# Kernel tuning notes

Hardware: AMD Instinct MI355X
Metric: run time of the kernel (lower is better)

Reference implementation:

```python
import jax, jax.numpy as jnp
import numpy as np

N, E = 50000, 800000
IN_DIM, HIDDEN, LATENT = 128, 256, 64


def setup_inputs() -> dict:
    key = jax.random.key(0)
    ks = jax.random.split(key, 10)
    def lin(k, fan_in, fan_out):
        s = 1.0 / np.sqrt(fan_in)
        return jax.random.uniform(k, (fan_in, fan_out), jnp.float32, -s, s)
    x = jax.random.normal(ks[0], (N, IN_DIM), jnp.float32)
    edge_index = jax.random.randint(ks[1], (2, E), 0, N, jnp.int64)
    return {
        "x": x,
        "edge_index": edge_index,
        # enc1: SAGEConv(in_dim, hidden): lin_l (neighbors, with bias), lin_r (root, no bias)
        "W1l": lin(ks[2], IN_DIM, HIDDEN),
        "b1": jnp.zeros((HIDDEN,), jnp.float32),
        "W1r": lin(ks[3], IN_DIM, HIDDEN),
        # enc2: SAGEConv(hidden, latent)
        "W2l": lin(ks[4], HIDDEN, LATENT),
        "b2": jnp.zeros((LATENT,), jnp.float32),
        "W2r": lin(ks[5], HIDDEN, LATENT),
        # decoder Linear(latent, in_dim)
        "Wd": lin(ks[6], LATENT, IN_DIM),
        "bd": jax.random.uniform(ks[7], (IN_DIM,), jnp.float32, -1.0 / np.sqrt(LATENT), 1.0 / np.sqrt(LATENT)),
    }


def _sage_conv(x, src, dst, Wl, b, Wr, num_nodes):
    # PyG SAGEConv (aggr='mean'): out = lin_l(mean_{j in N(i)} x_j) + lin_r(x_i)
    summed = jax.ops.segment_sum(x[src], dst, num_segments=num_nodes)   # [N, d]
    cnt = jax.ops.segment_sum(jnp.ones((src.shape[0],), x.dtype), dst, num_segments=num_nodes)
    mean = summed / jnp.maximum(cnt, 1.0)[:, None]
    return mean @ Wl + b + x @ Wr


def reference(x, edge_index, W1l, b1, W1r, W2l, b2, W2r, Wd, bd):
    src, dst = edge_index[0], edge_index[1]
    n = x.shape[0]
    h = jax.nn.relu(_sage_conv(x, src, dst, W1l, b1, W1r, n))
    z = _sage_conv(h, src, dst, W2l, b2, W2r, n)
    x_hat = z @ Wd + bd
    return (z, x_hat)
```

## Files before the change

kernel.cpp:

```cpp
#include <hip/hip_runtime.h>
#include <stdint.h>

#define NN 50000
#define NE 800000
#define NB 196
#define NBK 196
#define NBUK 196
#define CHK 4096
#define MTOT (NBUK * NBK)
#define MSB 151
#define CVTB 6250
#define PREPB 418

typedef __bf16 bf16x8 __attribute__((ext_vector_type(8)));
typedef float f32x4 __attribute__((ext_vector_type(4)));
typedef unsigned short ushort_t;

__device__ inline float bf2f(uint16_t u) {
    union { uint32_t i; float f; } v; v.i = ((uint32_t)u) << 16; return v.f;
}
__device__ inline uint16_t f2bf(float f) {
    uint32_t u = __float_as_uint(f);
    u += 0x7fffu + ((u >> 16) & 1u);
    return (uint16_t)(u >> 16);
}
__device__ inline float rdf(const void* p, int i, int bf) {
    return bf ? bf2f(((const ushort_t*)p)[i]) : ((const float*)p)[i];
}

__global__ __launch_bounds__(256) void k_modes(const int* __restrict__ ei, const ushort_t* __restrict__ xw,
                                               int* __restrict__ mode, int* __restrict__ fmode) {
    __shared__ int nz, bad;
    if (threadIdx.x == 0) { nz = 0; bad = 0; }
    __syncthreads();
    int t = threadIdx.x;
    int v = ei[2 * t + 1] | ei[2 * (t + 256) + 1] | ei[2 * (t + 512) + 1] | ei[2 * (t + 768) + 1];
    if (v) atomicOr(&nz, 1);
#pragma unroll
    for (int r = 0; r < 2; ++r) {
        uint16_t w = xw[t + 256 * r];
        int e = (w >> 7) & 0xFF;
        if (!(w == 0 || (e >= 96 && e <= 144))) atomicOr(&bad, 1);
    }
    __syncthreads();
    if (t == 0) { *mode = (nz == 0) ? 1 : 0; *fmode = (bad == 0) ? 1 : 0; }
}

__global__ __launch_bounds__(256) void k_stage1(const int* __restrict__ ei, const void* __restrict__ x,
                                                const void* __restrict__ W1l, const void* __restrict__ W1r,
                                                const void* __restrict__ W2l, const void* __restrict__ W2r,
                                                const void* __restrict__ Wd,
                                                const void* __restrict__ b1, const void* __restrict__ b2,
                                                const void* __restrict__ bd,
                                                const int* __restrict__ mode, const int* __restrict__ fmode,
                                                int* __restrict__ cntm, ushort_t* __restrict__ xb,
                                                ushort_t* __restrict__ wt, ushort_t* __restrict__ w2lt,
                                                ushort_t* __restrict__ w2rt, ushort_t* __restrict__ wdt,
                                                float* __restrict__ b1f, float* __restrict__ b2f,
                                                float* __restrict__ bdf) {
    int b = blockIdx.x, t = threadIdx.x;
    if (b < NBK) {
        __shared__ int hist[NBUK];
        if (t < NBUK) hist[t] = 0;
        __syncthreads();
        int sh = *mode;
        for (int i = t; i < CHK; i += 256) {
            int e = b * CHK + i;
            if (e < NE) {
                int d = ei[(size_t)(NE + e) << sh];
                atomicAdd(&hist[d >> 8], 1);
            }
        }
        __syncthreads();
        if (t < NBUK) cntm[t * NBK + b] = hist[t];
    } else if (b < NBK + CVTB) {
        int i = (b - NBK) * 256 + t;
        if (*fmode) {
            reinterpret_cast<ushort4*>(xb)[i] = reinterpret_cast<const ushort4*>(x)[i];
        } else {
            float4 v = reinterpret_cast<const float4*>(x)[i];
            ushort4 o;
            o.x = f2bf(v.x); o.y = f2bf(v.y); o.z = f2bf(v.z); o.w = f2bf(v.w);
            reinterpret_cast<ushort4*>(xb)[i] = o;
        }
    } else {
        int idx = (b - NBK - CVTB) * 256 + t;
        int bf = *fmode;
        if (idx < 65536) {
            int c = idx >> 8, k = idx & 255;
            float v = (k < 128) ? rdf(W1l, k * 256 + c, bf) : rdf(W1r, (k - 128) * 256 + c, bf);
            wt[c * 256 + k] = f2bf(v);
        } else if (idx < 81920) {
            int t2 = idx - 65536;
            int c = t2 >> 8, k = t2 & 255;
            w2lt[c * 256 + k] = f2bf(rdf(W2l, k * 64 + c, bf));
        } else if (idx < 98304) {
            int t2 = idx - 81920;
            int c = t2 >> 8, k = t2 & 255;
            w2rt[c * 256 + k] = f2bf(rdf(W2r, k * 64 + c, bf));
        } else if (idx < 106496) {
            int t2 = idx - 98304;
            int c = t2 >> 6, k = t2 & 63;
            wdt[c * 64 + k] = f2bf(rdf(Wd, k * 128 + c, bf));
        } else if (idx < 106752) {
            b1f[idx - 106496] = rdf(b1, idx - 106496, bf);
        } else if (idx < 106816) {
            b2f[idx - 106752] = rdf(b2, idx - 106752, bf);
        } else if (idx < 106944) {
            bdf[idx - 106816] = rdf(bd, idx - 106816, bf);
        }
    }
}

__device__ inline int block_scan256(int v, int* ws, int* btot) {
    int lane = threadIdx.x & 63, wv = threadIdx.x >> 6;
    int incl = v;
#pragma unroll
    for (int d = 1; d < 64; d <<= 1) {
        int n = __shfl_up(incl, d);
        if (lane >= d) incl += n;
    }
    if (lane == 63) ws[wv] = incl;
    __syncthreads();
    if (threadIdx.x == 0) {
        int r = 0;
#pragma unroll
        for (int k = 0; k < 4; ++k) { int t = ws[k]; ws[k] = r; r += t; }
        *btot = r;
    }
    __syncthreads();
    return ws[wv] + incl - v;
}

__global__ __launch_bounds__(256) void k_scanMA(const int* __restrict__ cntm, int* __restrict__ offm,
                                                int* __restrict__ bsM) {
    __shared__ int ws[4]; __shared__ int btot;
    int i = blockIdx.x * 256 + threadIdx.x;
    int v = (i < MTOT) ? cntm[i] : 0;
    int excl = block_scan256(v, ws, &btot);
    if (i < MTOT) offm[i] = excl;
    if (threadIdx.x == 0) bsM[blockIdx.x] = btot;
}
__global__ __launch_bounds__(256) void k_scanMB(const int* __restrict__ bsM, int* __restrict__ boM) {
    __shared__ int ws[4]; __shared__ int btot;
    int t = threadIdx.x;
    int v = (t < MSB) ? bsM[t] : 0;
    int excl = block_scan256(v, ws, &btot);
    if (t < MSB) boM[t] = excl;
}
__global__ __launch_bounds__(256) void k_scanMC(int* __restrict__ offm, const int* __restrict__ boM) {
    int i = blockIdx.x * 256 + threadIdx.x;
    if (i < MTOT) offm[i] += boM[blockIdx.x];
}

__global__ __launch_bounds__(256) void k_scatterC(const int* __restrict__ ei, const int* __restrict__ mode,
                                                  const int* __restrict__ offm, uint32_t* __restrict__ pairs) {
    __shared__ int cur[NBUK];
    int t = threadIdx.x, blk = blockIdx.x;
    if (t < NBUK) cur[t] = offm[t * NBK + blk];
    __syncthreads();
    int sh = *mode;
    for (int i = t; i < CHK; i += 256) {
        int e = blk * CHK + i;
        if (e < NE) {
            int s = ei[(size_t)e << sh];
            int d = ei[(size_t)(NE + e) << sh];
            int pos = atomicAdd(&cur[d >> 8], 1);
            pairs[pos] = (uint32_t)s | ((uint32_t)(d & 255) << 16);
        }
    }
}

__global__ __launch_bounds__(256) void k_d1(const uint32_t* __restrict__ pairs, const int* __restrict__ offm,
                                            int* __restrict__ deg) {
    __shared__ int hist[256];
    int t = threadIdx.x, b = blockIdx.x;
    hist[t] = 0;
    __syncthreads();
    int beg = offm[b * NBK];
    int end = (b + 1 < NBUK) ? offm[(b + 1) * NBK] : NE;
    for (int i = beg + t; i < end; i += 256) {
        uint32_t p = pairs[i];
        atomicAdd(&hist[p >> 16], 1);
    }
    __syncthreads();
    int node = b * 256 + t;
    if (node < NN) deg[node] = hist[t];
}

__global__ __launch_bounds__(256) void k_scanA(const int* __restrict__ deg, int* __restrict__ rowptr,
                                               int* __restrict__ blocksum) {
    __shared__ int ws[4]; __shared__ int btot;
    int i = blockIdx.x * 256 + threadIdx.x;
    int v = (i < NN) ? deg[i] : 0;
    int excl = block_scan256(v, ws, &btot);
    if (i < NN) rowptr[i] = excl;
    if (threadIdx.x == 0) blocksum[blockIdx.x] = btot;
}
__global__ __launch_bounds__(256) void k_scanB(const int* __restrict__ blocksum, int* __restrict__ blockoff,
                                               int* __restrict__ rowptr) {
    __shared__ int ws[4]; __shared__ int btot;
    int t = threadIdx.x;
    int v = (t < NB) ? blocksum[t] : 0;
    int excl = block_scan256(v, ws, &btot);
    if (t < NB) blockoff[t] = excl;
    if (t == NB - 1) rowptr[NN] = excl + v;
}
__global__ __launch_bounds__(256) void k_scanC(int* __restrict__ rowptr, const int* __restrict__ blockoff) {
    int i = blockIdx.x * 256 + threadIdx.x;
    if (i < NN) rowptr[i] += blockoff[blockIdx.x];
}

__global__ __launch_bounds__(256) void k_d2(const uint32_t* __restrict__ pairs, const int* __restrict__ offm,
                                            const int* __restrict__ rowptr, ushort_t* __restrict__ srclist) {
    __shared__ int cur[256];
    int t = threadIdx.x, b = blockIdx.x;
    int node = b * 256 + t;
    cur[t] = (node < NN) ? rowptr[node] : 0;
    __syncthreads();
    int beg = offm[b * NBK];
    int end = (b + 1 < NBUK) ? offm[(b + 1) * NBK] : NE;
    for (int i = beg + t; i < end; i += 256) {
        uint32_t p = pairs[i];
        int pos = atomicAdd(&cur[p >> 16], 1);
        srclist[pos] = (ushort_t)(p & 0xffff);
    }
}

__global__ __launch_bounds__(256) void k_agg128(const ushort_t* __restrict__ xb, const int* __restrict__ rowptr,
                                                const ushort_t* __restrict__ srclist, ushort_t* __restrict__ out) {
    int node = (blockIdx.x * 256 + threadIdx.x) >> 6;
    int lane = threadIdx.x & 63;
    if (node >= NN) return;
    int beg = rowptr[node], end = rowptr[node + 1];
    float a0 = 0.f, a1 = 0.f;
    int j = beg;
    for (; j + 7 < end; j += 8) {
        uint32_t p[8];
#pragma unroll
        for (int u = 0; u < 8; ++u) {
            int s = srclist[j + u];
            p[u] = *reinterpret_cast<const uint32_t*>(xb + (size_t)s * 128 + lane * 2);
        }
#pragma unroll
        for (int u = 0; u < 8; ++u) {
            a0 += bf2f((uint16_t)(p[u] & 0xffff));
            a1 += bf2f((uint16_t)(p[u] >> 16));
        }
    }
    for (; j + 3 < end; j += 4) {
        uint32_t p[4];
#pragma unroll
        for (int u = 0; u < 4; ++u) {
            int s = srclist[j + u];
            p[u] = *reinterpret_cast<const uint32_t*>(xb + (size_t)s * 128 + lane * 2);
        }
#pragma unroll
        for (int u = 0; u < 4; ++u) {
            a0 += bf2f((uint16_t)(p[u] & 0xffff));
            a1 += bf2f((uint16_t)(p[u] >> 16));
        }
    }
    for (; j < end; ++j) {
        int s = srclist[j];
        uint32_t p = *reinterpret_cast<const uint32_t*>(xb + (size_t)s * 128 + lane * 2);
        a0 += bf2f((uint16_t)(p & 0xffff));
        a1 += bf2f((uint16_t)(p >> 16));
    }
    float inv = 1.0f / (float)max(end - beg, 1);
    uint32_t o = (uint32_t)f2bf(a0 * inv) | ((uint32_t)f2bf(a1 * inv) << 16);
    *reinterpret_cast<uint32_t*>(out + (size_t)node * 128 + lane * 2) = o;
}

__global__ __launch_bounds__(256, 2) void k_gemm1p(const ushort_t* __restrict__ meanx, const ushort_t* __restrict__ xb,
                                                   const ushort_t* __restrict__ wt, const float* __restrict__ b1f,
                                                   ushort_t* __restrict__ h) {
    int wv = threadIdx.x >> 6, lane = threadIdx.x & 63;
    int m = lane & 15, q = lane >> 4;
    bf16x8 B[8][4];
#pragma unroll
    for (int ks = 0; ks < 8; ++ks) {
        int kb = ks * 32 + q * 8;
#pragma unroll
        for (int ct = 0; ct < 4; ++ct)
            B[ks][ct] = *reinterpret_cast<const bf16x8*>(wt + (size_t)(wv * 64 + ct * 16 + m) * 256 + kb);
    }
    const int ntiles = NN / 16;
    for (int t = blockIdx.x; t < ntiles; t += gridDim.x) {
        int r0 = t * 16;
        int row = r0 + m;
        f32x4 acc[4];
#pragma unroll
        for (int ct = 0; ct < 4; ++ct) acc[ct] = (f32x4){0.f, 0.f, 0.f, 0.f};
#pragma unroll
        for (int ks = 0; ks < 8; ++ks) {
            int kb = ks * 32 + q * 8;
            const ushort_t* ap = (ks < 4) ? (meanx + (size_t)row * 128 + kb)
                                          : (xb + (size_t)row * 128 + (kb - 128));
            bf16x8 a = *reinterpret_cast<const bf16x8*>(ap);
#pragma unroll
            for (int ct = 0; ct < 4; ++ct)
                acc[ct] = __builtin_amdgcn_mfma_f32_16x16x32_bf16(a, B[ks][ct], acc[ct], 0, 0, 0);
        }
#pragma unroll
        for (int ct = 0; ct < 4; ++ct) {
            int c = wv * 64 + ct * 16 + m;
            float bias = b1f[c];
#pragma unroll
            for (int i = 0; i < 4; ++i) {
                int rr = r0 + q * 4 + i;
                h[(size_t)rr * 256 + c] = f2bf(fmaxf(acc[ct][i] + bias, 0.f));
            }
        }
    }
}

__global__ __launch_bounds__(256, 2) void k_gemm2p(const ushort_t* __restrict__ h,
                                                   const ushort_t* __restrict__ w2lt, const ushort_t* __restrict__ w2rt,
                                                   const float* __restrict__ b2f,
                                                   ushort_t* __restrict__ y, float* __restrict__ r) {
    int wv = threadIdx.x >> 6, lane = threadIdx.x & 63;
    int m = lane & 15, q = lane >> 4;
    int op = wv >> 1;
    int cb = (wv & 1) * 32;
    const ushort_t* wtx = op ? w2rt : w2lt;
    bf16x8 B[8][2];
#pragma unroll
    for (int ks = 0; ks < 8; ++ks) {
        int kb = ks * 32 + q * 8;
#pragma unroll
        for (int ct = 0; ct < 2; ++ct)
            B[ks][ct] = *reinterpret_cast<const bf16x8*>(wtx + (size_t)(cb + ct * 16 + m) * 256 + kb);
    }
    const int ntiles = NN / 16;
    for (int t = blockIdx.x; t < ntiles; t += gridDim.x) {
        int r0 = t * 16;
        int row = r0 + m;
        f32x4 acc[2];
        acc[0] = (f32x4){0.f, 0.f, 0.f, 0.f}; acc[1] = acc[0];
#pragma unroll
        for (int ks = 0; ks < 8; ++ks) {
            int kb = ks * 32 + q * 8;
            bf16x8 a = *reinterpret_cast<const bf16x8*>(h + (size_t)row * 256 + kb);
#pragma unroll
            for (int ct = 0; ct < 2; ++ct)
                acc[ct] = __builtin_amdgcn_mfma_f32_16x16x32_bf16(a, B[ks][ct], acc[ct], 0, 0, 0);
        }
#pragma unroll
        for (int ct = 0; ct < 2; ++ct) {
            int c = cb + ct * 16 + m;
#pragma unroll
            for (int i = 0; i < 4; ++i) {
                int rr = r0 + q * 4 + i;
                if (op == 0) y[(size_t)rr * 64 + c] = f2bf(acc[ct][i]);
                else         r[(size_t)rr * 64 + c] = acc[ct][i] + b2f[c];
            }
        }
    }
}

__global__ __launch_bounds__(256) void k_agg2y(const ushort_t* __restrict__ y, const int* __restrict__ rowptr,
                                               const ushort_t* __restrict__ srclist, const float* __restrict__ r,
                                               float* __restrict__ zf, ushort_t* __restrict__ zb) {
    int node = (blockIdx.x * 256 + threadIdx.x) >> 6;
    int lane = threadIdx.x & 63;
    if (node >= NN) return;
    int half = lane >> 5, l32 = lane & 31;
    int beg = rowptr[node], end = rowptr[node + 1];
    float a0 = 0.f, a1 = 0.f;
    int j = beg + half;
    for (; j + 6 < end; j += 8) {
        uint32_t p[4];
#pragma unroll
        for (int u = 0; u < 4; ++u) {
            int s = srclist[j + 2 * u];
            p[u] = *reinterpret_cast<const uint32_t*>(y + (size_t)s * 64 + l32 * 2);
        }
#pragma unroll
        for (int u = 0; u < 4; ++u) {
            a0 += bf2f((uint16_t)(p[u] & 0xffff));
            a1 += bf2f((uint16_t)(p[u] >> 16));
        }
    }
    for (; j < end; j += 2) {
        int s = srclist[j];
        uint32_t p = *reinterpret_cast<const uint32_t*>(y + (size_t)s * 64 + l32 * 2);
        a0 += bf2f((uint16_t)(p & 0xffff));
        a1 += bf2f((uint16_t)(p >> 16));
    }
    a0 += __shfl_xor(a0, 32);
    a1 += __shfl_xor(a1, 32);
    if (half == 0) {
        float inv = 1.0f / (float)max(end - beg, 1);
        float2 rv = *reinterpret_cast<const float2*>(r + (size_t)node * 64 + l32 * 2);
        float z0 = a0 * inv + rv.x;
        float z1 = a1 * inv + rv.y;
        float2 zo; zo.x = z0; zo.y = z1;
        *reinterpret_cast<float2*>(zf + (size_t)node * 64 + l32 * 2) = zo;
        uint32_t o = (uint32_t)f2bf(z0) | ((uint32_t)f2bf(z1) << 16);
        *reinterpret_cast<uint32_t*>(zb + (size_t)node * 64 + l32 * 2) = o;
    }
}

__global__ __launch_bounds__(256, 2) void k_gemm3p(const ushort_t* __restrict__ zb, const ushort_t* __restrict__ wdt,
                                                   const float* __restrict__ bdf, float* __restrict__ xhat) {
    int wv = threadIdx.x >> 6, lane = threadIdx.x & 63;
    int m = lane & 15, q = lane >> 4;
    bf16x8 B[2][2];
#pragma unroll
    for (int ks = 0; ks < 2; ++ks) {
        int kb = ks * 32 + q * 8;
#pragma unroll
        for (int ct = 0; ct < 2; ++ct)
            B[ks][ct] = *reinterpret_cast<const bf16x8*>(wdt + (size_t)(wv * 32 + ct * 16 + m) * 64 + kb);
    }
    const int ntiles = NN / 16;
    for (int t = blockIdx.x; t < ntiles; t += gridDim.x) {
        int r0 = t * 16;
        int row = r0 + m;
        f32x4 acc[2];
        acc[0] = (f32x4){0.f, 0.f, 0.f, 0.f}; acc[1] = acc[0];
#pragma unroll
        for (int ks = 0; ks < 2; ++ks) {
            int kb = ks * 32 + q * 8;
            bf16x8 a = *reinterpret_cast<const bf16x8*>(zb + (size_t)row * 64 + kb);
#pragma unroll
            for (int ct = 0; ct < 2; ++ct)
                acc[ct] = __builtin_amdgcn_mfma_f32_16x16x32_bf16(a, B[ks][ct], acc[ct], 0, 0, 0);
        }
#pragma unroll
        for (int ct = 0; ct < 2; ++ct) {
            int c = wv * 32 + ct * 16 + m;
            float bias = bdf[c];
#pragma unroll
            for (int i = 0; i < 4; ++i) {
                int rr = r0 + q * 4 + i;
                xhat[(size_t)rr * 128 + c] = acc[ct][i] + bias;
            }
        }
    }
}

extern "C" void kernel_launch(void* const* d_in, const int* in_sizes, int n_in,
                              void* d_out, int out_size, void* d_ws, size_t ws_size,
                              hipStream_t stream) {
    const void *px = nullptr, *pei = nullptr, *pW1l = nullptr, *pW1r = nullptr,
               *pW2l = nullptr, *pW2r = nullptr, *pWd = nullptr,
               *pb1 = nullptr, *pb2 = nullptr, *pbd = nullptr;
    for (int i = 0; i < n_in; ++i) {
        const void* p = d_in[i];
        switch (in_sizes[i]) {
            case 6400000: px  = p; break;
            case 1600000: pei = p; break;
            case 32768:   if (!pW1l) pW1l = p; else pW1r = p; break;
            case 16384:   if (!pW2l) pW2l = p; else pW2r = p; break;
            case 8192:    pWd = p; break;
            case 256:     pb1 = p; break;
            case 128:     pbd = p; break;
            case 64:      pb2 = p; break;
            default: break;
        }
    }
    if (!px || !pei || !pW1l || !pW1r || !pW2l || !pW2r || !pWd || !pb1 || !pb2 || !pbd) {
        px = d_in[0]; pei = d_in[1]; pW1l = d_in[2]; pb1 = d_in[3]; pW1r = d_in[4];
        pW2l = d_in[5]; pb2 = d_in[6]; pW2r = d_in[7]; pWd = d_in[8]; pbd = d_in[9];
    }
    const int* ei = (const int*)pei;

    char* base = (char*)d_ws;
    size_t off = 0;
    auto alloc = [&](size_t bytes) -> void* {
        void* r = base + off;
        off = (off + bytes + 255) & ~(size_t)255;
        return r;
    };
    int* mode     = (int*)alloc(4);
    int* fmode    = (int*)alloc(4);
    int* rowptr   = (int*)alloc((size_t)(NN + 1) * 4);
    int* blocksum = (int*)alloc((size_t)NB * 4);
    int* blockoff = (int*)alloc((size_t)NB * 4);
    int* cntm     = (int*)alloc((size_t)MTOT * 4);
    int* offm     = (int*)alloc((size_t)MTOT * 4);
    int* bsM      = (int*)alloc(256 * 4);
    int* boM      = (int*)alloc(256 * 4);
    ushort_t* srclist = (ushort_t*)alloc((size_t)NE * 2);
    ushort_t* wt   = (ushort_t*)alloc((size_t)65536 * 2);
    ushort_t* w2lt = (ushort_t*)alloc((size_t)16384 * 2);
    ushort_t* w2rt = (ushort_t*)alloc((size_t)16384 * 2);
    ushort_t* wdt  = (ushort_t*)alloc((size_t)8192 * 2);
    float* b1f    = (float*)alloc(256 * 4);
    float* b2f    = (float*)alloc(64 * 4);
    float* bdf    = (float*)alloc(128 * 4);
    ushort_t* xb  = (ushort_t*)alloc((size_t)NN * 128 * 2);
    ushort_t* h   = (ushort_t*)alloc((size_t)NN * 256 * 2);

    uint32_t* pairs = (uint32_t*)h;
    int* deg        = (int*)((char*)h + (size_t)NE * 4 + 256);

    float* out_z    = (float*)d_out;
    float* out_xhat = out_z + (size_t)NN * 64;

    ushort_t* meanx = (ushort_t*)out_xhat;
    float*    rbuf  = (float*)((char*)out_xhat + (size_t)NN * 128 * 2);
    ushort_t* y     = xb;
    ushort_t* zb    = xb + (size_t)NN * 64;

    k_modes<<<1, 256, 0, stream>>>(ei, (const ushort_t*)px, mode, fmode);

    k_stage1<<<NBK + CVTB + PREPB, 256, 0, stream>>>(ei, px, pW1l, pW1r, pW2l, pW2r, pWd, pb1, pb2, pbd,
                                                     mode, fmode, cntm, xb, wt, w2lt, w2rt, wdt,
                                                     b1f, b2f, bdf);

    k_scanMA<<<MSB, 256, 0, stream>>>(cntm, offm, bsM);
    k_scanMB<<<1, 256, 0, stream>>>(bsM, boM);
    k_scanMC<<<MSB, 256, 0, stream>>>(offm, boM);
    k_scatterC<<<NBK, 256, 0, stream>>>(ei, mode, offm, pairs);
    k_d1<<<NBUK, 256, 0, stream>>>(pairs, offm, deg);
    k_scanA<<<NB, 256, 0, stream>>>(deg, rowptr, blocksum);
    k_scanB<<<1, 256, 0, stream>>>(blocksum, blockoff, rowptr);
    k_scanC<<<NB, 256, 0, stream>>>(rowptr, blockoff);
    k_d2<<<NBUK, 256, 0, stream>>>(pairs, offm, rowptr, srclist);

    int ab = (NN + 3) / 4;
    k_agg128<<<ab, 256, 0, stream>>>(xb, rowptr, srclist, meanx);

    k_gemm1p<<<512, 256, 0, stream>>>(meanx, xb, wt, b1f, h);
    k_gemm2p<<<512, 256, 0, stream>>>(h, w2lt, w2rt, b2f, y, rbuf);
    k_agg2y<<<ab, 256, 0, stream>>>(y, rowptr, srclist, rbuf, out_z, zb);
    k_gemm3p<<<512, 256, 0, stream>>>(zb, wdt, bdf, out_xhat);
}
```

Measured before the change: 252.5 us.

## Fuse launch chain: inline mode detection, merge scans, fuse second aggregation with decoder

Removes the separate mode-detection kernel by having each block redundantly detect index width and input dtype. Each three-kernel scan is collapsed to two by having every block reduce the preceding block sums itself, and the degree histogram is fused with the first-level scan. The layer-2 aggregation is fused with the decoder GEMM through an LDS tile, and z is written in place over the root-term buffer. The goal is fewer launches and less intermediate traffic, at the cost of redundant per-block detection reads and reductions.

```diff
diff --git a/kernel.cpp b/kernel.cpp
--- a/kernel.cpp
+++ b/kernel.cpp
@@ -28,22 +28,28 @@
     return bf ? bf2f(((const ushort_t*)p)[i]) : ((const float*)p)[i];
 }
 
-__global__ __launch_bounds__(256) void k_modes(const int* __restrict__ ei, const ushort_t* __restrict__ xw,
-                                               int* __restrict__ mode, int* __restrict__ fmode) {
-    __shared__ int nz, bad;
-    if (threadIdx.x == 0) { nz = 0; bad = 0; }
-    __syncthreads();
+__device__ inline int blk_or(int v, int* flag) {
+    if (threadIdx.x == 0) *flag = 0;
+    __syncthreads();
+    if (v) atomicOr(flag, 1);
+    __syncthreads();
+    return *flag;
+}
+__device__ inline int detect_sh(const int* __restrict__ ei, int* flag) {
     int t = threadIdx.x;
     int v = ei[2 * t + 1] | ei[2 * (t + 256) + 1] | ei[2 * (t + 512) + 1] | ei[2 * (t + 768) + 1];
-    if (v) atomicOr(&nz, 1);
+    return blk_or(v, flag) ? 0 : 1;
+}
+__device__ inline int detect_bf(const ushort_t* __restrict__ xw, int* flag) {
+    int t = threadIdx.x;
+    int bad = 0;
 #pragma unroll
     for (int r = 0; r < 2; ++r) {
         uint16_t w = xw[t + 256 * r];
         int e = (w >> 7) & 0xFF;
-        if (!(w == 0 || (e >= 96 && e <= 144))) atomicOr(&bad, 1);
-    }
-    __syncthreads();
-    if (t == 0) { *mode = (nz == 0) ? 1 : 0; *fmode = (bad == 0) ? 1 : 0; }
+        if (!(w == 0 || (e >= 96 && e <= 144))) bad = 1;
+    }
+    return blk_or(bad, flag) ? 0 : 1;
 }
 
 __global__ __launch_bounds__(256) void k_stage1(const int* __restrict__ ei, const void* __restrict__ x,
@@ -52,18 +58,18 @@
                                                 const void* __restrict__ Wd,
                                                 const void* __restrict__ b1, const void* __restrict__ b2,
                                                 const void* __restrict__ bd,
-                                                const int* __restrict__ mode, const int* __restrict__ fmode,
                                                 int* __restrict__ cntm, ushort_t* __restrict__ xb,
                                                 ushort_t* __restrict__ wt, ushort_t* __restrict__ w2lt,
                                                 ushort_t* __restrict__ w2rt, ushort_t* __restrict__ wdt,
                                                 float* __restrict__ b1f, float* __restrict__ b2f,
                                                 float* __restrict__ bdf) {
+    __shared__ int flag;
     int b = blockIdx.x, t = threadIdx.x;
     if (b < NBK) {
+        int sh = detect_sh(ei, &flag);
         __shared__ int hist[NBUK];
         if (t < NBUK) hist[t] = 0;
         __syncthreads();
-        int sh = *mode;
         for (int i = t; i < CHK; i += 256) {
             int e = b * CHK + i;
             if (e < NE) {
@@ -74,8 +80,9 @@
         __syncthreads();
         if (t < NBUK) cntm[t * NBK + b] = hist[t];
     } else if (b < NBK + CVTB) {
+        int bf = detect_bf((const ushort_t*)x, &flag);
         int i = (b - NBK) * 256 + t;
-        if (*fmode) {
+        if (bf) {
             reinterpret_cast<ushort4*>(xb)[i] = reinterpret_cast<const ushort4*>(x)[i];
         } else {
             float4 v = reinterpret_cast<const float4*>(x)[i];
@@ -84,8 +91,8 @@
             reinterpret_cast<ushort4*>(xb)[i] = o;
         }
     } else {
+        int bf = detect_bf((const ushort_t*)x, &flag);
         int idx = (b - NBK - CVTB) * 256 + t;
-        int bf = *fmode;
         if (idx < 65536) {
             int c = idx >> 8, k = idx & 255;
             float v = (k < 128) ? rdf(W1l, k * 256 + c, bf) : rdf(W1r, (k - 128) * 256 + c, bf);
@@ -141,25 +148,30 @@
     if (i < MTOT) offm[i] = excl;
     if (threadIdx.x == 0) bsM[blockIdx.x] = btot;
 }
-__global__ __launch_bounds__(256) void k_scanMB(const int* __restrict__ bsM, int* __restrict__ boM) {
-    __shared__ int ws[4]; __shared__ int btot;
-    int t = threadIdx.x;
-    int v = (t < MSB) ? bsM[t] : 0;
-    int excl = block_scan256(v, ws, &btot);
-    if (t < MSB) boM[t] = excl;
-}
-__global__ __launch_bounds__(256) void k_scanMC(int* __restrict__ offm, const int* __restrict__ boM) {
-    int i = blockIdx.x * 256 + threadIdx.x;
-    if (i < MTOT) offm[i] += boM[blockIdx.x];
-}
-
-__global__ __launch_bounds__(256) void k_scatterC(const int* __restrict__ ei, const int* __restrict__ mode,
+
+__global__ __launch_bounds__(256) void k_scanMC2(int* __restrict__ offm, const int* __restrict__ bsM) {
+    __shared__ int red[256];
+    int t = threadIdx.x, b = blockIdx.x;
+    red[t] = (t < b) ? bsM[t] : 0;
+    __syncthreads();
+#pragma unroll
+    for (int s = 128; s > 0; s >>= 1) {
+        if (t < s) red[t] += red[t + s];
+        __syncthreads();
+    }
+    int boff = red[0];
+    int i = b * 256 + t;
+    if (i < MTOT) offm[i] += boff;
+}
+
+__global__ __launch_bounds__(256) void k_scatterC(const int* __restrict__ ei,
                                                   const int* __restrict__ offm, uint32_t* __restrict__ pairs) {
     __shared__ int cur[NBUK];
+    __shared__ int flag;
     int t = threadIdx.x, blk = blockIdx.x;
+    int sh = detect_sh(ei, &flag);
     if (t < NBUK) cur[t] = offm[t * NBK + blk];
     __syncthreads();
-    int sh = *mode;
     for (int i = t; i < CHK; i += 256) {
         int e = blk * CHK + i;
         if (e < NE) {
@@ -171,9 +183,10 @@
     }
 }
 
-__global__ __launch_bounds__(256) void k_d1(const uint32_t* __restrict__ pairs, const int* __restrict__ offm,
-                                            int* __restrict__ deg) {
+__global__ __launch_bounds__(256) void k_d1s(const uint32_t* __restrict__ pairs, const int* __restrict__ offm,
+                                             int* __restrict__ rowptr, int* __restrict__ blocksum) {
     __shared__ int hist[256];
+    __shared__ int ws[4]; __shared__ int btot;
     int t = threadIdx.x, b = blockIdx.x;
     hist[t] = 0;
     __syncthreads();
@@ -184,31 +197,27 @@
         atomicAdd(&hist[p >> 16], 1);
     }
     __syncthreads();
+    int v = hist[t];
+    int excl = block_scan256(v, ws, &btot);
     int node = b * 256 + t;
-    if (node < NN) deg[node] = hist[t];
-}
-
-__global__ __launch_bounds__(256) void k_scanA(const int* __restrict__ deg, int* __restrict__ rowptr,
-                                               int* __restrict__ blocksum) {
-    __shared__ int ws[4]; __shared__ int btot;
-    int i = blockIdx.x * 256 + threadIdx.x;
-    int v = (i < NN) ? deg[i] : 0;
-    int excl = block_scan256(v, ws, &btot);
-    if (i < NN) rowptr[i] = excl;
-    if (threadIdx.x == 0) blocksum[blockIdx.x] = btot;
-}
-__global__ __launch_bounds__(256) void k_scanB(const int* __restrict__ blocksum, int* __restrict__ blockoff,
-                                               int* __restrict__ rowptr) {
-    __shared__ int ws[4]; __shared__ int btot;
-    int t = threadIdx.x;
-    int v = (t < NB) ? blocksum[t] : 0;
-    int excl = block_scan256(v, ws, &btot);
-    if (t < NB) blockoff[t] = excl;
-    if (t == NB - 1) rowptr[NN] = excl + v;
-}
-__global__ __launch_bounds__(256) void k_scanC(int* __restrict__ rowptr, const int* __restrict__ blockoff) {
-    int i = blockIdx.x * 256 + threadIdx.x;
-    if (i < NN) rowptr[i] += blockoff[blockIdx.x];
+    if (node < NN) rowptr[node] = excl;
+    if (t == 0) blocksum[b] = btot;
+}
+
+__global__ __launch_bounds__(256) void k_scanC2(int* __restrict__ rowptr, const int* __restrict__ blocksum) {
+    __shared__ int red[256];
+    int t = threadIdx.x, b = blockIdx.x;
+    red[t] = (t < b && t < NB) ? blocksum[t] : 0;
+    __syncthreads();
+#pragma unroll
+    for (int s = 128; s > 0; s >>= 1) {
+        if (t < s) red[t] += red[t + s];
+        __syncthreads();
+    }
+    int boff = red[0];
+    int i = b * 256 + t;
+    if (i < NN) rowptr[i] += boff;
+    if (b == 0 && t == 0) rowptr[NN] = NE;
 }
 
 __global__ __launch_bounds__(256) void k_d2(const uint32_t* __restrict__ pairs, const int* __restrict__ offm,
@@ -359,51 +368,13 @@
     }
 }
 
-__global__ __launch_bounds__(256) void k_agg2y(const ushort_t* __restrict__ y, const int* __restrict__ rowptr,
-                                               const ushort_t* __restrict__ srclist, const float* __restrict__ r,
-                                               float* __restrict__ zf, ushort_t* __restrict__ zb) {
-    int node = (blockIdx.x * 256 + threadIdx.x) >> 6;
-    int lane = threadIdx.x & 63;
-    if (node >= NN) return;
-    int half = lane >> 5, l32 = lane & 31;
-    int beg = rowptr[node], end = rowptr[node + 1];
-    float a0 = 0.f, a1 = 0.f;
-    int j = beg + half;
-    for (; j + 6 < end; j += 8) {
-        uint32_t p[4];
-#pragma unroll
-        for (int u = 0; u < 4; ++u) {
-            int s = srclist[j + 2 * u];
-            p[u] = *reinterpret_cast<const uint32_t*>(y + (size_t)s * 64 + l32 * 2);
-        }
-#pragma unroll
-        for (int u = 0; u < 4; ++u) {
-            a0 += bf2f((uint16_t)(p[u] & 0xffff));
-            a1 += bf2f((uint16_t)(p[u] >> 16));
-        }
-    }
-    for (; j < end; j += 2) {
-        int s = srclist[j];
-        uint32_t p = *reinterpret_cast<const uint32_t*>(y + (size_t)s * 64 + l32 * 2);
-        a0 += bf2f((uint16_t)(p & 0xffff));
-        a1 += bf2f((uint16_t)(p >> 16));
-    }
-    a0 += __shfl_xor(a0, 32);
-    a1 += __shfl_xor(a1, 32);
-    if (half == 0) {
-        float inv = 1.0f / (float)max(end - beg, 1);
-        float2 rv = *reinterpret_cast<const float2*>(r + (size_t)node * 64 + l32 * 2);
-        float z0 = a0 * inv + rv.x;
-        float z1 = a1 * inv + rv.y;
-        float2 zo; zo.x = z0; zo.y = z1;
-        *reinterpret_cast<float2*>(zf + (size_t)node * 64 + l32 * 2) = zo;
-        uint32_t o = (uint32_t)f2bf(z0) | ((uint32_t)f2bf(z1) << 16);
-        *reinterpret_cast<uint32_t*>(zb + (size_t)node * 64 + l32 * 2) = o;
-    }
-}
-
-__global__ __launch_bounds__(256, 2) void k_gemm3p(const ushort_t* __restrict__ zb, const ushort_t* __restrict__ wdt,
-                                                   const float* __restrict__ bdf, float* __restrict__ xhat) {
+__global__ __launch_bounds__(256) void k_agg2g3(const ushort_t* __restrict__ y, const int* __restrict__ rowptr,
+                                                const ushort_t* __restrict__ srclist,
+                                                float* zr,
+                                                const ushort_t* __restrict__ wdt, const float* __restrict__ bdf,
+                                                float* __restrict__ xhat) {
+    __shared__ alignas(16) ushort_t zt[16][72];
+    int b = blockIdx.x;
     int wv = threadIdx.x >> 6, lane = threadIdx.x & 63;
     int m = lane & 15, q = lane >> 4;
     bf16x8 B[2][2];
@@ -414,29 +385,65 @@
         for (int ct = 0; ct < 2; ++ct)
             B[ks][ct] = *reinterpret_cast<const bf16x8*>(wdt + (size_t)(wv * 32 + ct * 16 + m) * 64 + kb);
     }
-    const int ntiles = NN / 16;
-    for (int t = blockIdx.x; t < ntiles; t += gridDim.x) {
-        int r0 = t * 16;
-        int row = r0 + m;
-        f32x4 acc[2];
-        acc[0] = (f32x4){0.f, 0.f, 0.f, 0.f}; acc[1] = acc[0];
-#pragma unroll
-        for (int ks = 0; ks < 2; ++ks) {
-            int kb = ks * 32 + q * 8;
-            bf16x8 a = *reinterpret_cast<const bf16x8*>(zb + (size_t)row * 64 + kb);
-#pragma unroll
-            for (int ct = 0; ct < 2; ++ct)
-                acc[ct] = __builtin_amdgcn_mfma_f32_16x16x32_bf16(a, B[ks][ct], acc[ct], 0, 0, 0);
-        }
-#pragma unroll
-        for (int ct = 0; ct < 2; ++ct) {
-            int c = wv * 32 + ct * 16 + m;
-            float bias = bdf[c];
-#pragma unroll
-            for (int i = 0; i < 4; ++i) {
-                int rr = r0 + q * 4 + i;
-                xhat[(size_t)rr * 128 + c] = acc[ct][i] + bias;
+    float bias0 = bdf[wv * 32 + m], bias1 = bdf[wv * 32 + 16 + m];
+
+    int half = lane >> 5, l32 = lane & 31;
+#pragma unroll
+    for (int s = 0; s < 4; ++s) {
+        int node = b * 16 + wv * 4 + s;
+        int beg = rowptr[node], end = rowptr[node + 1];
+        float a0 = 0.f, a1 = 0.f;
+        int j = beg + half;
+        for (; j + 6 < end; j += 8) {
+            uint32_t p[4];
+#pragma unroll
+            for (int u = 0; u < 4; ++u) {
+                int sx = srclist[j + 2 * u];
+                p[u] = *reinterpret_cast<const uint32_t*>(y + (size_t)sx * 64 + l32 * 2);
             }
+#pragma unroll
+            for (int u = 0; u < 4; ++u) {
+                a0 += bf2f((uint16_t)(p[u] & 0xffff));
+                a1 += bf2f((uint16_t)(p[u] >> 16));
+            }
+        }
+        for (; j < end; j += 2) {
+            int sx = srclist[j];
+            uint32_t p = *reinterpret_cast<const uint32_t*>(y + (size_t)sx * 64 + l32 * 2);
+            a0 += bf2f((uint16_t)(p & 0xffff));
+            a1 += bf2f((uint16_t)(p >> 16));
+        }
+        a0 += __shfl_xor(a0, 32);
+        a1 += __shfl_xor(a1, 32);
+        if (half == 0) {
+            float inv = 1.0f / (float)max(end - beg, 1);
+            float2 rv = *reinterpret_cast<const float2*>(zr + (size_t)node * 64 + l32 * 2);
+            float z0 = a0 * inv + rv.x;
+            float z1 = a1 * inv + rv.y;
+            float2 zo; zo.x = z0; zo.y = z1;
+            *reinterpret_cast<float2*>(zr + (size_t)node * 64 + l32 * 2) = zo;
+            uint32_t o = (uint32_t)f2bf(z0) | ((uint32_t)f2bf(z1) << 16);
+            *reinterpret_cast<uint32_t*>(&zt[wv * 4 + s][l32 * 2]) = o;
+        }
+    }
+    __syncthreads();
+    f32x4 acc[2];
+    acc[0] = (f32x4){0.f, 0.f, 0.f, 0.f}; acc[1] = acc[0];
+#pragma unroll
+    for (int ks = 0; ks < 2; ++ks) {
+        bf16x8 a = *reinterpret_cast<const bf16x8*>(&zt[m][ks * 32 + q * 8]);
+#pragma unroll
+        for (int ct = 0; ct < 2; ++ct)
+            acc[ct] = __builtin_amdgcn_mfma_f32_16x16x32_bf16(a, B[ks][ct], acc[ct], 0, 0, 0);
+    }
+#pragma unroll
+    for (int ct = 0; ct < 2; ++ct) {
+        int c = wv * 32 + ct * 16 + m;
+        float bb = ct ? bias1 : bias0;
+#pragma unroll
+        for (int i = 0; i < 4; ++i) {
+            int rr = b * 16 + q * 4 + i;
+            xhat[(size_t)rr * 128 + c] = acc[ct][i] + bb;
         }
     }
 }
@@ -474,15 +481,11 @@
         off = (off + bytes + 255) & ~(size_t)255;
         return r;
     };
-    int* mode     = (int*)alloc(4);
-    int* fmode    = (int*)alloc(4);
     int* rowptr   = (int*)alloc((size_t)(NN + 1) * 4);
     int* blocksum = (int*)alloc((size_t)NB * 4);
-    int* blockoff = (int*)alloc((size_t)NB * 4);
     int* cntm     = (int*)alloc((size_t)MTOT * 4);
     int* offm     = (int*)alloc((size_t)MTOT * 4);
     int* bsM      = (int*)alloc(256 * 4);
-    int* boM      = (int*)alloc(256 * 4);
     ushort_t* srclist = (ushort_t*)alloc((size_t)NE * 2);
     ushort_t* wt   = (ushort_t*)alloc((size_t)65536 * 2);
     ushort_t* w2lt = (ushort_t*)alloc((size_t)16384 * 2);
@@ -495,30 +498,22 @@
     ushort_t* h   = (ushort_t*)alloc((size_t)NN * 256 * 2);
 
     uint32_t* pairs = (uint32_t*)h;
-    int* deg        = (int*)((char*)h + (size_t)NE * 4 + 256);
 
     float* out_z    = (float*)d_out;
     float* out_xhat = out_z + (size_t)NN * 64;
 
     ushort_t* meanx = (ushort_t*)out_xhat;
-    float*    rbuf  = (float*)((char*)out_xhat + (size_t)NN * 128 * 2);
     ushort_t* y     = xb;
-    ushort_t* zb    = xb + (size_t)NN * 64;
-
-    k_modes<<<1, 256, 0, stream>>>(ei, (const ushort_t*)px, mode, fmode);
+    float*    rbuf  = out_z;
 
     k_stage1<<<NBK + CVTB + PREPB, 256, 0, stream>>>(ei, px, pW1l, pW1r, pW2l, pW2r, pWd, pb1, pb2, pbd,
-                                                     mode, fmode, cntm, xb, wt, w2lt, w2rt, wdt,
-                                                     b1f, b2f, bdf);
+                                                     cntm, xb, wt, w2lt, w2rt, wdt, b1f, b2f, bdf);
 
     k_scanMA<<<MSB, 256, 0, stream>>>(cntm, offm, bsM);
-    k_scanMB<<<1, 256, 0, stream>>>(bsM, boM);
-    k_scanMC<<<MSB, 256, 0, stream>>>(offm, boM);
-    k_scatterC<<<NBK, 256, 0, stream>>>(ei, mode, offm, pairs);
-    k_d1<<<NBUK, 256, 0, stream>>>(pairs, offm, deg);
-    k_scanA<<<NB, 256, 0, stream>>>(deg, rowptr, blocksum);
-    k_scanB<<<1, 256, 0, stream>>>(blocksum, blockoff, rowptr);
-    k_scanC<<<NB, 256, 0, stream>>>(rowptr, blockoff);
+    k_scanMC2<<<MSB, 256, 0, stream>>>(offm, bsM);
+    k_scatterC<<<NBK, 256, 0, stream>>>(ei, offm, pairs);
+    k_d1s<<<NBUK, 256, 0, stream>>>(pairs, offm, rowptr, blocksum);
+    k_scanC2<<<NB, 256, 0, stream>>>(rowptr, blocksum);
     k_d2<<<NBUK, 256, 0, stream>>>(pairs, offm, rowptr, srclist);
 
     int ab = (NN + 3) / 4;
@@ -526,6 +521,5 @@
 
     k_gemm1p<<<512, 256, 0, stream>>>(meanx, xb, wt, b1f, h);
     k_gemm2p<<<512, 256, 0, stream>>>(h, w2lt, w2rt, b2f, y, rbuf);
-    k_agg2y<<<ab, 256, 0, stream>>>(y, rowptr, srclist, rbuf, out_z, zb);
-    k_gemm3p<<<512, 256, 0, stream>>>(zb, wdt, bdf, out_xhat);
-}
+    k_agg2g3<<<NN / 16, 256, 0, stream>>>(y, rowptr, srclist, rbuf, wdt, bdf, out_xhat);
+}
```

New measurement: 248.9 us. No clear change (-1.4%).
